# Performance work log

Measured on AMD Instinct MI355X. Metric: run time of the kernel, lower is better.

Reference implementation:

```python
import jax, jax.numpy as jnp
import numpy as np

EPS = 1e-5

def mean_variance_norm(x):
    # x: [b, c, h, w]; per-(b,c) instance norm over spatial, unbiased var (torch default)
    b, c, h, w = x.shape
    xf = x.reshape(b, c, h * w)
    mean = xf.mean(axis=2)
    var = xf.var(axis=2, ddof=1) + EPS
    std = jnp.sqrt(var)
    return (x - mean[:, :, None, None]) / std[:, :, None, None]

def conv1x1(x, w, b):
    # w: [out_c, in_c], b: [out_c]
    return jnp.einsum('oc,bchw->bohw', w, x) + b[None, :, None, None]

def setup_inputs() -> dict:
    key = jax.random.key(0)
    ks = jax.random.split(key, 10)
    b, C, H, W = 4, 512, 64, 64
    content = jax.random.normal(ks[0], (b, C, H, W), dtype=jnp.float32)
    style = jax.random.normal(ks[1], (b, C, H, W), dtype=jnp.float32)
    def w_(k, o, i):
        return jax.random.normal(k, (o, i), dtype=jnp.float32) * 0.02
    def b_(k, o):
        return jax.random.normal(k, (o,), dtype=jnp.float32) * 0.02
    return {
        'content': content, 'style': style,
        'f_w': w_(ks[2], C, C), 'f_b': b_(ks[3], C),
        'g_w': w_(ks[4], C, C), 'g_b': b_(ks[5], C),
        'h_w': w_(ks[6], C, C), 'h_b': b_(ks[7], C),
        'out_w': w_(ks[8], C, C), 'out_b': b_(ks[9], C),
    }

def reference(content, style, f_w, f_b, g_w, g_b, h_w, h_b, out_w, out_b):
    b, C, h, w = content.shape
    F = conv1x1(mean_variance_norm(content), f_w, f_b)   # [b,C,h,w]
    G = conv1x1(mean_variance_norm(style), g_w, g_b)     # [b,C,hg,wg]
    H = conv1x1(style, h_w, h_b)                          # [b,C,hg,wg]
    # spatial <= max_sample, so no subsampling branch
    Gf = G.reshape(b, C, -1)                              # [b,C,M]
    Hf = H.reshape(b, C, -1)                              # [b,C,M]
    Ff = F.reshape(b, C, -1)                              # [b,C,N]
    S = jnp.einsum('bcn,bcm->bnm', Ff, Gf)                # [b,N,M]
    S = jax.nn.softmax(S, axis=-1)
    styled = jnp.einsum('bcm,bnm->bcn', Hf, S)            # [b,C,N]
    styled = styled.reshape(b, C, h, w)
    return conv1x1(styled, out_w, out_b)
```

## Files before the change

kernel.cpp:

```cpp
#include <hip/hip_runtime.h>
#include <hip/hip_bf16.h>

typedef _Float16 f16;
typedef __attribute__((ext_vector_type(8))) _Float16 half8;
typedef __attribute__((ext_vector_type(4))) _Float16 half4;
typedef __attribute__((ext_vector_type(4))) float f32x4;

#define AS1 __attribute__((address_space(1)))
#define AS3 __attribute__((address_space(3)))

constexpr int CH  = 512;
constexpr int NSP = 4096;
constexpr int NB  = 4;

#define VM8  asm volatile("s_waitcnt vmcnt(8)"  ::: "memory")
#define VM6  asm volatile("s_waitcnt vmcnt(6)"  ::: "memory")
#define VM4  asm volatile("s_waitcnt vmcnt(4)"  ::: "memory")
#define VM2  asm volatile("s_waitcnt vmcnt(2)"  ::: "memory")
#define VM0  asm volatile("s_waitcnt vmcnt(0)"  ::: "memory")
#define BARS do { __builtin_amdgcn_s_barrier(); asm volatile("" ::: "memory"); } while (0)
#define SP1  __builtin_amdgcn_s_setprio(1)
#define SP0  __builtin_amdgcn_s_setprio(0)

__device__ __forceinline__ void gload_lds16(const void* g, void* l) {
    __builtin_amdgcn_global_load_lds((const AS1 void*)g, (AS3 void*)l, 16, 0, 0);
}

__global__ void transpose_f16_kernel(const float* __restrict__ content, const float* __restrict__ style,
                                     f16* __restrict__ content_t, f16* __restrict__ style_t,
                                     float* __restrict__ raw)
{
    int b = blockIdx.z & 3, is_style = blockIdx.z >> 2;
    const float* src = (is_style ? style : content) + (size_t)b * CH * NSP;
    f16* dst = (is_style ? style_t : content_t) + (size_t)b * NSP * CH;
    int c0 = blockIdx.y * 64, n0 = blockIdx.x * 64;
    __shared__ f16 tile[64][72];
    int t = threadIdx.x;
    #pragma unroll
    for (int i = 0; i < 4; i++) {
        int idx = t + i*256;
        int cr = idx >> 4, n4 = (idx & 15) * 4;
        float4 v = *(const float4*)(src + (size_t)(c0+cr)*NSP + n0 + n4);
        tile[cr][n4+0] = (f16)v.x; tile[cr][n4+1] = (f16)v.y;
        tile[cr][n4+2] = (f16)v.z; tile[cr][n4+3] = (f16)v.w;
    }
    __syncthreads();
    {
        int row = t >> 2, seg = (t & 3) * 16;
        float s1 = 0.f, s2 = 0.f;
        #pragma unroll
        for (int j = 0; j < 16; j++) {
            float x = (float)tile[row][seg + j];
            s1 += x; s2 += x * x;
        }
        s1 += __shfl_down(s1, 2, 4); s1 += __shfl_down(s1, 1, 4);
        s2 += __shfl_down(s2, 2, 4); s2 += __shfl_down(s2, 1, 4);
        if ((t & 3) == 0) {
            int si = is_style * 2 * NB * CH + b * CH + c0 + row;
            atomicAdd(&raw[si], s1);
            atomicAdd(&raw[si + NB * CH], s2);
        }
    }
    int nr = t >> 2, seg = (t & 3) * 16;
    __align__(16) f16 out_v[16];
    #pragma unroll
    for (int j = 0; j < 16; j++) out_v[j] = tile[seg + j][nr];
    f16* dp = dst + (size_t)(n0+nr)*CH + c0 + seg;
    *(int4*)dp = ((int4*)out_v)[0];
    *(int4*)(dp + 8) = ((int4*)out_v)[1];
}

__global__ void effw_kernel(const float* __restrict__ fw, const float* __restrict__ fb,
                            const float* __restrict__ gw, const float* __restrict__ gb,
                            const float* __restrict__ hw, const float* __restrict__ ow,
                            const float* __restrict__ raw,
                            f16* __restrict__ fw_e, float* __restrict__ fb_e,
                            f16* __restrict__ gw_e, float* __restrict__ gb_e,
                            f16* __restrict__ hw_h, f16* __restrict__ ow_h)
{
    int o = blockIdx.x, b = blockIdx.y, mode = blockIdx.z, t = threadIdx.x;
    if (mode >= 2) {
        if (b != 0) return;
        const float* srcw = (mode == 2) ? hw : ow;
        f16* dstw = (mode == 2) ? hw_h : ow_h;
        for (int c = t; c < CH; c += 128) dstw[o*CH + c] = (f16)srcw[o*CH + c];
        return;
    }
    const float* w  = mode ? gw : fw;
    const float* rw = raw + (mode ? 2*NB*CH : 0);
    f16* we = mode ? gw_e : fw_e;
    float part = 0.f;
    for (int c = t; c < CH; c += 128) {
        float s1 = rw[b*CH + c], s2 = rw[NB*CH + b*CH + c];
        float mn = s1 * (1.f/NSP);
        float var = (s2 - (float)NSP*mn*mn) * (1.f/(NSP-1));
        float is = rsqrtf(var + 1e-5f);
        float wv = w[o*CH + c];
        we[((size_t)b*CH + o)*CH + c] = (f16)(wv * is);
        part += wv * mn * is;
    }
    #pragma unroll
    for (int off = 32; off; off >>= 1) part += __shfl_down(part, off);
    __shared__ float rr[2];
    if ((t & 63) == 0) rr[t >> 6] = part;
    __syncthreads();
    if (t == 0) (mode ? gb_e : fb_e)[b*CH + o] = (mode ? gb : fb)[o] - (rr[0] + rr[1]);
}

__global__ __launch_bounds__(256)
void conv3_kernel(const f16* __restrict__ fw_e, const float* __restrict__ fb_e,
                  const f16* __restrict__ gw_e, const float* __restrict__ gb_e,
                  const f16* __restrict__ hw_h, const float* __restrict__ h_b,
                  const f16* __restrict__ content_t, const f16* __restrict__ style_t,
                  f16* __restrict__ F_t, f16* __restrict__ G_t, f16* __restrict__ H_)
{
    const int T = gridDim.x;
    const int bid = blockIdx.x;
    const int tile = (bid & 7) * (T >> 3) + (bid >> 3);
    const int zz = tile >> 7, rem = tile & 127;
    const int mt = rem >> 5, nt = rem & 31;
    const int kind = zz >> 2, b = zz & 3;

    const f16* W; const float* bias; const f16* Xt; f16* Y;
    if (kind == 0)      { W = fw_e + (size_t)b*CH*CH; bias = fb_e + b*CH; Xt = content_t + (size_t)b*NSP*CH; Y = F_t + (size_t)b*NSP*CH; }
    else if (kind == 1) { W = gw_e + (size_t)b*CH*CH; bias = gb_e + b*CH; Xt = style_t + (size_t)b*NSP*CH; Y = G_t + (size_t)b*NSP*CH; }
    else                { W = hw_h;                    bias = h_b;         Xt = style_t + (size_t)b*NSP*CH; Y = H_ + (size_t)b*CH*NSP; }

    const int m0 = mt * 128, n0 = nt * 128;
    const int t = threadIdx.x, wave = t >> 6, lane = t & 63;
    const int l15 = lane & 15, l4 = lane >> 4;
    const int wm = (wave >> 1) * 64, wn = (wave & 1) * 64;

    __shared__ __align__(16) f16 Al[8192];
    __shared__ __align__(16) f16 Bl[8192];

    f32x4 acc[4][4] = {};

    for (int ks = 0; ks < CH/64; ks++) {
        const int kk = ks * 64;
        #pragma unroll
        for (int j = 0; j < 4; j++) {
            int L  = ((wave*4 + j)*64 + lane) * 16;
            int SL = L ^ (((L >> 7) & 7) << 4);
            int row = SL >> 7, seg = (SL & 127) >> 1;
            gload_lds16(W  + (size_t)(m0 + row)*CH + kk + seg, &Al[L >> 1]);
            gload_lds16(Xt + (size_t)(n0 + row)*CH + kk + seg, &Bl[L >> 1]);
        }
        VM0; BARS;
        #pragma unroll
        for (int kb = 0; kb < 2; kb++) {
            half8 a[4], bb[4];
            #pragma unroll
            for (int i = 0; i < 4; i++) {
                int ab = (wm + i*16 + l15)*128 + kb*64 + l4*16;
                ab ^= ((ab >> 7) & 7) << 4;
                a[i] = *(const half8*)&Al[ab >> 1];
                int bby = (wn + i*16 + l15)*128 + kb*64 + l4*16;
                bby ^= ((bby >> 7) & 7) << 4;
                bb[i] = *(const half8*)&Bl[bby >> 1];
            }
            #pragma unroll
            for (int i = 0; i < 4; i++)
                #pragma unroll
                for (int jj = 0; jj < 4; jj++)
                    acc[i][jj] = __builtin_amdgcn_mfma_f32_16x16x32_f16(a[i], bb[jj], acc[i][jj], 0, 0, 0);
        }
        BARS;
    }

    #pragma unroll
    for (int i = 0; i < 4; i++) {
        const int ob = m0 + wm + i*16 + l4*4;
        f32x4 bv = *(const f32x4*)(bias + ob);
        #pragma unroll
        for (int jj = 0; jj < 4; jj++) {
            const int n = n0 + wn + jj*16 + l15;
            f32x4 v = acc[i][jj];
            v[0] += bv[0]; v[1] += bv[1]; v[2] += bv[2]; v[3] += bv[3];
            if (kind < 2) {
                half4 pk; pk[0]=(f16)v[0]; pk[1]=(f16)v[1]; pk[2]=(f16)v[2]; pk[3]=(f16)v[3];
                *(half4*)(Y + (size_t)n * CH + ob) = pk;
            } else {
                #pragma unroll
                for (int r = 0; r < 4; r++) Y[(size_t)(ob + r) * NSP + n] = (f16)v[r];
            }
        }
    }
}

template<int MODE>
__global__ __launch_bounds__(256)
void gemm_kernel(const f16* __restrict__ W, long wstrideb,
                 const f16* __restrict__ Xt, long xstrideb,
                 const float* __restrict__ bias, long bstrideb,
                 void* __restrict__ Y, long ystrideb,
                 int K, long ostride)
{
    const int z = blockIdx.z;
    W    += (size_t)z * wstrideb;
    Xt   += (size_t)z * xstrideb;
    bias += (size_t)z * bstrideb;
    const int m0 = blockIdx.y * 128, n0 = blockIdx.x * 128;
    const int t = threadIdx.x, wave = t >> 6, lane = t & 63;
    const int l15 = lane & 15, l4 = lane >> 4;
    const int wm = (wave >> 1) * 64, wn = (wave & 1) * 64;

    __shared__ __align__(16) f16 Al[2][8192];
    __shared__ __align__(16) f16 Bl[2][8192];

    f32x4 acc[4][4] = {};

    auto stage = [&](int bufi, int kk) {
        #pragma unroll
        for (int j = 0; j < 4; j++) {
            int L  = ((wave*4 + j)*64 + lane) * 16;
            int SL = L ^ (((L >> 7) & 7) << 4);
            int row = SL >> 7, seg = (SL & 127) >> 1;
            gload_lds16(W  + (size_t)(m0 + row)*K + kk + seg, &Al[bufi][L >> 1]);
            gload_lds16(Xt + (size_t)(n0 + row)*K + kk + seg, &Bl[bufi][L >> 1]);
        }
    };

    const int nks = K >> 6;
    stage(0, 0);
    for (int ks = 0; ks < nks; ks++) {
        int bufi = ks & 1;
        if (ks < nks-1) { stage(bufi ^ 1, (ks + 1) * 64); VM8; }
        else            { VM0; }
        BARS;
        #pragma unroll
        for (int kb = 0; kb < 2; kb++) {
            half8 a[4], bb[4];
            #pragma unroll
            for (int i = 0; i < 4; i++) {
                int ab = (wm + i*16 + l15)*128 + kb*64 + l4*16;
                ab ^= ((ab >> 7) & 7) << 4;
                a[i] = *(const half8*)&Al[bufi][ab >> 1];
                int bby = (wn + i*16 + l15)*128 + kb*64 + l4*16;
                bby ^= ((bby >> 7) & 7) << 4;
                bb[i] = *(const half8*)&Bl[bufi][bby >> 1];
            }
            #pragma unroll
            for (int i = 0; i < 4; i++)
                #pragma unroll
                for (int jj = 0; jj < 4; jj++)
                    acc[i][jj] = __builtin_amdgcn_mfma_f32_16x16x32_f16(a[i], bb[jj], acc[i][jj], 0, 0, 0);
        }
        BARS;
    }

    #pragma unroll
    for (int i = 0; i < 4; i++) {
        const int ob = m0 + wm + i*16 + l4*4;
        f32x4 bv = *(const f32x4*)(bias + ob);
        #pragma unroll
        for (int jj = 0; jj < 4; jj++) {
            const int n = n0 + wn + jj*16 + l15;
            f32x4 v = acc[i][jj];
            v[0] += bv[0]; v[1] += bv[1]; v[2] += bv[2]; v[3] += bv[3];
            float* Yf = (float*)Y + (size_t)z * ystrideb;
            #pragma unroll
            for (int r = 0; r < 4; r++) Yf[(size_t)(ob + r) * ostride + n] = v[r];
        }
    }
}

__global__ __launch_bounds__(256)
void out_fused_kernel(const f16* __restrict__ W, const f16* __restrict__ P0, const f16* __restrict__ P1,
                      const float* __restrict__ bias, float* __restrict__ Y)
{
    const int z = blockIdx.z;
    const f16* p0 = P0 + (size_t)z * NSP * CH;
    const f16* p1 = P1 + (size_t)z * NSP * CH;
    float* Yf = Y + (size_t)z * CH * NSP;
    const int m0 = blockIdx.y * 128, n0 = blockIdx.x * 128;
    const int t = threadIdx.x, wave = t >> 6, lane = t & 63;
    const int l15 = lane & 15, l4 = lane >> 4;
    const int wm = (wave >> 1) * 64, wn = (wave & 1) * 64;

    __shared__ __align__(16) f16 Al[8192];
    __shared__ __align__(16) f16 Bl[8192];

    f32x4 acc[4][4] = {};

    for (int ks = 0; ks < CH/64; ks++) {
        const int kk = ks * 64;
        int Ls[4];
        half8 b0[4], b1[4];
        #pragma unroll
        for (int j = 0; j < 4; j++) {
            int L  = ((wave*4 + j)*64 + lane) * 16;
            int SL = L ^ (((L >> 7) & 7) << 4);
            int row = SL >> 7, seg = (SL & 127) >> 1;
            gload_lds16(W + (size_t)(m0 + row)*CH + kk + seg, &Al[L >> 1]);
            b0[j] = *(const half8*)(p0 + (size_t)(n0 + row)*CH + kk + seg);
            b1[j] = *(const half8*)(p1 + (size_t)(n0 + row)*CH + kk + seg);
            Ls[j] = L;
        }
        #pragma unroll
        for (int j = 0; j < 4; j++) {
            half8 s;
            #pragma unroll
            for (int e = 0; e < 8; e++) s[e] = (f16)((float)b0[j][e] + (float)b1[j][e]);
            *(half8*)&Bl[Ls[j] >> 1] = s;
        }
        __syncthreads();
        #pragma unroll
        for (int kb = 0; kb < 2; kb++) {
            half8 a[4], bb[4];
            #pragma unroll
            for (int i = 0; i < 4; i++) {
                int ab = (wm + i*16 + l15)*128 + kb*64 + l4*16;
                ab ^= ((ab >> 7) & 7) << 4;
                a[i] = *(const half8*)&Al[ab >> 1];
                int bby = (wn + i*16 + l15)*128 + kb*64 + l4*16;
                bby ^= ((bby >> 7) & 7) << 4;
                bb[i] = *(const half8*)&Bl[bby >> 1];
            }
            #pragma unroll
            for (int i = 0; i < 4; i++)
                #pragma unroll
                for (int jj = 0; jj < 4; jj++)
                    acc[i][jj] = __builtin_amdgcn_mfma_f32_16x16x32_f16(a[i], bb[jj], acc[i][jj], 0, 0, 0);
        }
        __syncthreads();
    }

    #pragma unroll
    for (int i = 0; i < 4; i++) {
        const int ob = m0 + wm + i*16 + l4*4;
        f32x4 bv = *(const f32x4*)(bias + ob);
        #pragma unroll
        for (int jj = 0; jj < 4; jj++) {
            const int n = n0 + wn + jj*16 + l15;
            f32x4 v = acc[i][jj];
            #pragma unroll
            for (int r = 0; r < 4; r++) Yf[(size_t)(ob + r) * NSP + n] = v[r] + bv[r];
        }
    }
}

template<int TPB, int NCT>
__global__ __launch_bounds__(256)
void gemm_att_kernel(const f16* __restrict__ W, long wstrideb,
                     const f16* __restrict__ Xt, long xstrideb,
                     f16* __restrict__ Y, long ystrideb,
                     int K, long ostride)
{
    const int T = gridDim.x;
    const int bid = blockIdx.x;
    const int tile = (bid & 7) * (T >> 3) + (bid >> 3);
    const int z = tile / TPB, rem = tile - z * TPB;
    const int mt = rem / NCT, nt = rem - mt * NCT;
    W  += (size_t)z * wstrideb;
    Xt += (size_t)z * xstrideb;
    f16* Yb = Y + (size_t)z * ystrideb;
    const int m0 = mt * 128, n0 = nt * 128;

    const int t = threadIdx.x, wave = t >> 6, lane = t & 63;
    const int l15 = lane & 15, l4 = lane >> 4;
    const int wm = (wave >> 1) * 64, wn = (wave & 1) * 64;

    __shared__ __align__(16) f16 Al[8192];
    __shared__ __align__(16) f16 Bl[8192];

    f32x4 acc[4][4] = {};

    const int nks = K >> 6;
    for (int ks = 0; ks < nks; ks++) {
        const int kk = ks * 64;
        #pragma unroll
        for (int j = 0; j < 4; j++) {
            int L  = ((wave*4 + j)*64 + lane) * 16;
            int SL = L ^ (((L >> 7) & 7) << 4);
            int row = SL >> 7, seg = (SL & 127) >> 1;
            gload_lds16(W  + (size_t)(m0 + row)*K + kk + seg, &Al[L >> 1]);
            gload_lds16(Xt + (size_t)(n0 + row)*K + kk + seg, &Bl[L >> 1]);
        }
        VM0; BARS;
        #pragma unroll
        for (int kb = 0; kb < 2; kb++) {
            half8 a[4], bb[4];
            #pragma unroll
            for (int i = 0; i < 4; i++) {
                int ab = (wm + i*16 + l15)*128 + kb*64 + l4*16;
                ab ^= ((ab >> 7) & 7) << 4;
                a[i] = *(const half8*)&Al[ab >> 1];
                int bby = (wn + i*16 + l15)*128 + kb*64 + l4*16;
                bby ^= ((bby >> 7) & 7) << 4;
                bb[i] = *(const half8*)&Bl[bby >> 1];
            }
            #pragma unroll
            for (int i = 0; i < 4; i++)
                #pragma unroll
                for (int jj = 0; jj < 4; jj++)
                    acc[i][jj] = __builtin_amdgcn_mfma_f32_16x16x32_f16(a[i], bb[jj], acc[i][jj], 0, 0, 0);
        }
        BARS;
    }

    #pragma unroll
    for (int i = 0; i < 4; i++) {
        const int ob = m0 + wm + i*16 + l4*4;
        #pragma unroll
        for (int jj = 0; jj < 4; jj++) {
            const int ncol = n0 + wn + jj*16 + l15;
            #pragma unroll
            for (int r = 0; r < 4; r++)
                Yb[(size_t)(ob + r) * ostride + ncol] = (f16)acc[i][jj][r];
        }
    }
}

template<int TPB, int NCT, int SPLITK>
__global__ __launch_bounds__(512)
void gemm256_kernel(const f16* __restrict__ W, long wstrideb,
                    const f16* __restrict__ Xt, long xstrideb,
                    f16* __restrict__ Y0, f16* __restrict__ Y1, long ystrideb,
                    int K, int kstride, long ostride)
{
    const int T = gridDim.x;
    const int bid = blockIdx.x;
    const int tile = (bid & 7) * (T >> 3) + (bid >> 3);
    int rem = tile, sp = 0;
    if constexpr (SPLITK == 2) { sp = tile / (NB * TPB); rem = tile - sp * NB * TPB; }
    const int z = rem / TPB; rem -= z * TPB;
    const int mt = rem / NCT, nt = rem - mt * NCT;
    const f16* Wb = W  + (size_t)z * wstrideb + (size_t)sp * K;
    const f16* Xb = Xt + (size_t)z * xstrideb + (size_t)sp * K;
    f16* Yb = ((SPLITK == 2 && sp) ? Y1 : Y0) + (size_t)z * ystrideb;
    const int m0 = mt * 256, n0 = nt * 256;

    const int t = threadIdx.x, lane = t & 63, wave = t >> 6;
    const int l15 = lane & 15, l4 = lane >> 4;
    const int wr = wave >> 2, wc = wave & 3;

    __shared__ __align__(16) f16 As[2][16384];
    __shared__ __align__(16) f16 Bs[2][16384];

    f32x4 acc[8][4] = {};

    auto stA = [&](int nbuf, int kk, int half, int q) {
        int L  = half*16384 + q*8192 + t*16;
        int SL = L ^ (((L >> 7) & 7) << 4);
        gload_lds16(Wb + (size_t)(m0 + (SL >> 7)) * kstride + kk + ((SL & 127) >> 1), &As[nbuf][L >> 1]);
    };
    auto stB = [&](int nbuf, int kk, int half, int q) {
        int L  = half*16384 + q*8192 + t*16;
        int SL = L ^ (((L >> 7) & 7) << 4);
        gload_lds16(Xb + (size_t)(n0 + (SL >> 7)) * kstride + kk + ((SL & 127) >> 1), &Bs[nbuf][L >> 1]);
    };
    auto ldA = [&](int buf, int i, int kb) {
        int L = (((i&3)*16) + wr*64 + ((i>>2)*128) + l15)*128 + kb*64 + l4*16;
        L ^= ((L >> 7) & 7) << 4;
        return *(const half8*)&As[buf][L >> 1];
    };
    auto ldB = [&](int buf, int j, int kb) {
        int L = (((j&1)*16) + wc*32 + ((j>>1)*128) + l15)*128 + kb*64 + l4*16;
        L ^= ((L >> 7) & 7) << 4;
        return *(const half8*)&Bs[buf][L >> 1];
    };

    const int nks = K >> 6;
    stA(0,0,0,0); stA(0,0,0,1);
    stB(0,0,0,0); stB(0,0,0,1);
    stB(0,0,1,0); stB(0,0,1,1);
    stA(0,0,1,0); stA(0,0,1,1);
    VM4;
    if (nks > 1) {
        stA(1,64,0,0); stA(1,64,0,1);
        stB(1,64,0,0); stB(1,64,0,1);
        stB(1,64,1,0); stB(1,64,1,1);
        VM6;
    } else { VM0; }
    BARS;

    half8 a[4][2], b01[2][2], b23[2][2];

    for (int kt = 0; kt < nks; kt++) {
        const int buf = kt & 1;
        const int kk1 = (kt+1) << 6, kk2 = (kt+2) << 6;
        const bool s1 = (kt+1 < nks), s2 = (kt+2 < nks);

        #pragma unroll
        for (int i = 0; i < 4; i++) { a[i][0] = ldA(buf, i, 0); a[i][1] = ldA(buf, i, 1); }
        #pragma unroll
        for (int j = 0; j < 2; j++) { b01[j][0] = ldB(buf, j, 0); b01[j][1] = ldB(buf, j, 1); }
        if (s1) { stA(buf^1, kk1, 1, 0); stA(buf^1, kk1, 1, 1); }
        else    { VM2; }
        BARS; SP1;
        #pragma unroll
        for (int i = 0; i < 4; i++)
            #pragma unroll
            for (int j = 0; j < 2; j++)
                #pragma unroll
                for (int kb = 0; kb < 2; kb++)
                    acc[i][j] = __builtin_amdgcn_mfma_f32_16x16x32_f16(a[i][kb], b01[j][kb], acc[i][j], 0, 0, 0);
        SP0; BARS;

        #pragma unroll
        for (int j = 0; j < 2; j++) { b23[j][0] = ldB(buf, 2+j, 0); b23[j][1] = ldB(buf, 2+j, 1); }
        if (s2)       { stA(buf, kk2, 0, 0); stA(buf, kk2, 0, 1); }
        else if (!s1) { VM0; }
        BARS; SP1;
        #pragma unroll
        for (int i = 0; i < 4; i++)
            #pragma unroll
            for (int j = 0; j < 2; j++)
                #pragma unroll
                for (int kb = 0; kb < 2; kb++)
                    acc[i][2+j] = __builtin_amdgcn_mfma_f32_16x16x32_f16(a[i][kb], b23[j][kb], acc[i][2+j], 0, 0, 0);
        SP0; BARS;

        #pragma unroll
        for (int i = 0; i < 4; i++) { a[i][0] = ldA(buf, 4+i, 0); a[i][1] = ldA(buf, 4+i, 1); }
        if (s2) { stB(buf, kk2, 0, 0); stB(buf, kk2, 0, 1); }
        BARS; SP1;
        #pragma unroll
        for (int i = 0; i < 4; i++)
            #pragma unroll
            for (int j = 0; j < 2; j++)
                #pragma unroll
                for (int kb = 0; kb < 2; kb++)
                    acc[4+i][2+j] = __builtin_amdgcn_mfma_f32_16x16x32_f16(a[i][kb], b23[j][kb], acc[4+i][2+j], 0, 0, 0);
        SP0; BARS;

        if (s2)      { stB(buf, kk2, 1, 0); stB(buf, kk2, 1, 1); VM6; }
        else if (s1) { VM4; }
        BARS; SP1;
        #pragma unroll
        for (int i = 0; i < 4; i++)
            #pragma unroll
            for (int j = 0; j < 2; j++)
                #pragma unroll
                for (int kb = 0; kb < 2; kb++)
                    acc[4+i][j] = __builtin_amdgcn_mfma_f32_16x16x32_f16(a[i][kb], b01[j][kb], acc[4+i][j], 0, 0, 0);
        SP0; BARS;
    }

    #pragma unroll
    for (int i = 0; i < 8; i++) {
        const int ob = m0 + ((i&3)*16) + wr*64 + ((i>>2)*128) + l4*4;
        #pragma unroll
        for (int j = 0; j < 4; j++) {
            const int ncol = n0 + ((j&1)*16) + wc*32 + ((j>>1)*128) + l15;
            f32x4 v = acc[i][j];
            #pragma unroll
            for (int r = 0; r < 4; r++)
                Yb[(size_t)(ob + r) * ostride + ncol] = (f16)v[r];
        }
    }
}

__global__ __launch_bounds__(256)
void softmax_kernel(f16* __restrict__ S, int nrows)
{
    int row = blockIdx.x * 4 + (threadIdx.x >> 6);
    if (row >= nrows) return;
    int lane = threadIdx.x & 63;
    f16* p = S + (size_t)row * NSP + lane * 8;

    half8 v[8];
    #pragma unroll
    for (int j = 0; j < 8; j++) v[j] = *(const half8*)(p + j * 512);

    float mx = -1e30f;
    #pragma unroll
    for (int j = 0; j < 8; j++)
        #pragma unroll
        for (int e = 0; e < 8; e++) mx = fmaxf(mx, (float)v[j][e]);
    #pragma unroll
    for (int off = 32; off; off >>= 1) mx = fmaxf(mx, __shfl_xor(mx, off));

    float ex[64];
    float s = 0.f;
    #pragma unroll
    for (int j = 0; j < 8; j++)
        #pragma unroll
        for (int e = 0; e < 8; e++) {
            float x = __expf((float)v[j][e] - mx);
            ex[j*8 + e] = x; s += x;
        }
    #pragma unroll
    for (int off = 32; off; off >>= 1) s += __shfl_xor(s, off);
    float inv = 1.0f / s;

    #pragma unroll
    for (int j = 0; j < 8; j++) {
        half8 o;
        #pragma unroll
        for (int e = 0; e < 8; e++) o[e] = (f16)(ex[j*8 + e] * inv);
        *(half8*)(p + j * 512) = o;
    }
}

extern "C" void kernel_launch(void* const* d_in, const int* in_sizes, int n_in,
                              void* d_out, int out_size, void* d_ws, size_t ws_size,
                              hipStream_t stream)
{
    const float* content = (const float*)d_in[0];
    const float* style   = (const float*)d_in[1];
    const float* f_w = (const float*)d_in[2];
    const float* f_b = (const float*)d_in[3];
    const float* g_w = (const float*)d_in[4];
    const float* g_b = (const float*)d_in[5];
    const float* h_w = (const float*)d_in[6];
    const float* h_b = (const float*)d_in[7];
    const float* o_w = (const float*)d_in[8];
    const float* o_b = (const float*)d_in[9];

    char* ws = (char*)d_ws;
    size_t off = 0;
    auto alloc = [&](size_t bytes) -> void* {
        void* p = ws + off;
        off += (bytes + 255) & ~(size_t)255;
        return p;
    };
    float* raw = (float*)alloc(4 * NB*CH * 4);
    f16* fw_e = (f16*)alloc((size_t)NB*CH*CH*2);
    f16* gw_e = (f16*)alloc((size_t)NB*CH*CH*2);
    f16* hw_h = (f16*)alloc((size_t)CH*CH*2);
    f16* ow_h = (f16*)alloc((size_t)CH*CH*2);
    float* fb_e = (float*)alloc((size_t)NB*CH*4);
    float* gb_e = (float*)alloc((size_t)NB*CH*4);
    f16* content_t = (f16*)alloc((size_t)NB*NSP*CH*2);
    f16* style_t   = (f16*)alloc((size_t)NB*NSP*CH*2);
    f16* F_t = (f16*)alloc((size_t)NB*NSP*CH*2);
    f16* G_t = (f16*)alloc((size_t)NB*NSP*CH*2);
    f16* H_  = (f16*)alloc((size_t)NB*CH*NSP*2);
    f16* styled_t = content_t;

    size_t s_plane = (size_t)NSP * NSP;
    bool all4 = (off + 4 * s_plane * 2 <= ws_size);
    f16* S16 = (f16*)alloc((all4 ? 4 : 1) * s_plane * 2);
    if (off > ws_size) return;

    hipMemsetAsync(raw, 0, 4 * NB*CH * 4, stream);
    transpose_f16_kernel<<<dim3(NSP/64, CH/64, NB*2), dim3(256), 0, stream>>>(
        content, style, content_t, style_t, raw);
    effw_kernel<<<dim3(CH, NB, 4), dim3(128), 0, stream>>>(f_w, f_b, g_w, g_b, h_w, o_w, raw,
                                                           fw_e, fb_e, gw_e, gb_e, hw_h, ow_h);
    conv3_kernel<<<dim3(12*128), dim3(256), 0, stream>>>(
        fw_e, fb_e, gw_e, gb_e, hw_h, h_b, content_t, style_t, F_t, G_t, H_);

    if (all4) {
        gemm256_kernel<256,16,1><<<dim3(1024), dim3(512), 0, stream>>>(
            F_t, (long)NSP*CH, G_t, (long)NSP*CH, S16, nullptr, (long)s_plane, CH, CH, (long)NSP);
        softmax_kernel<<<dim3(NB*NSP/4), dim3(256), 0, stream>>>(S16, NB*NSP);
        gemm256_kernel<32,2,2><<<dim3(256), dim3(512), 0, stream>>>(
            S16, (long)s_plane, H_, (long)CH*NSP, F_t, G_t, (long)NSP*CH, NSP/2, NSP, (long)CH);
        out_fused_kernel<<<dim3(NSP/128, CH/128, NB), dim3(256), 0, stream>>>(
            ow_h, F_t, G_t, o_b, (float*)d_out);
    } else {
        for (int b = 0; b < NB; b++) {
            gemm_att_kernel<1024,32><<<dim3(1024), dim3(256), 0, stream>>>(
                F_t + (size_t)b*NSP*CH, 0L, G_t + (size_t)b*NSP*CH, 0L,
                S16, 0L, CH, (long)NSP);
            softmax_kernel<<<dim3(NSP/4), dim3(256), 0, stream>>>(S16, NSP);
            gemm_att_kernel<128,4><<<dim3(128), dim3(256), 0, stream>>>(
                S16, 0L, H_ + (size_t)b*CH*NSP, 0L,
                styled_t + (size_t)b*NSP*CH, 0L, NSP, (long)CH);
        }
        gemm_kernel<2><<<dim3(NSP/128, CH/128, NB), dim3(256), 0, stream>>>(
            ow_h, 0L, styled_t, (long)NSP*CH, o_b, 0L, d_out, (long)CH*NSP, CH, (long)NSP);
    }
}
```

Baseline: 286.2 us.

## Fuse softmax exponentiation into PV GEMM and defer normalization to output

Replaces the in-place softmax pass with a read-only max/sum kernel that stores per-row max and inverse sum. The PV GEMM now applies exp(s - max) to the S tiles as it reads them from LDS, and the output projection multiplies by the inverse sum while combining the split-K partials. This removes the write-back of the full f16 S matrix, but adds many exp operations inside the GEMM's LDS-read path. That may slow the MFMA loop, and the unnormalized f16 accumulation changes precision.

```diff
diff --git a/kernel.cpp b/kernel.cpp
--- a/kernel.cpp
+++ b/kernel.cpp
@@ -267,11 +267,13 @@
 
 __global__ __launch_bounds__(256)
 void out_fused_kernel(const f16* __restrict__ W, const f16* __restrict__ P0, const f16* __restrict__ P1,
+                      const float* __restrict__ linv,
                       const float* __restrict__ bias, float* __restrict__ Y)
 {
     const int z = blockIdx.z;
     const f16* p0 = P0 + (size_t)z * NSP * CH;
     const f16* p1 = P1 + (size_t)z * NSP * CH;
+    const float* li = linv + (size_t)z * NSP;
     float* Yf = Y + (size_t)z * CH * NSP;
     const int m0 = blockIdx.y * 128, n0 = blockIdx.x * 128;
     const int t = threadIdx.x, wave = t >> 6, lane = t & 63;
@@ -287,6 +289,7 @@
         const int kk = ks * 64;
         int Ls[4];
         half8 b0[4], b1[4];
+        float lv[4];
         #pragma unroll
         for (int j = 0; j < 4; j++) {
             int L  = ((wave*4 + j)*64 + lane) * 16;
@@ -295,13 +298,14 @@
             gload_lds16(W + (size_t)(m0 + row)*CH + kk + seg, &Al[L >> 1]);
             b0[j] = *(const half8*)(p0 + (size_t)(n0 + row)*CH + kk + seg);
             b1[j] = *(const half8*)(p1 + (size_t)(n0 + row)*CH + kk + seg);
+            lv[j] = li[n0 + row];
             Ls[j] = L;
         }
         #pragma unroll
         for (int j = 0; j < 4; j++) {
             half8 s;
             #pragma unroll
-            for (int e = 0; e < 8; e++) s[e] = (f16)((float)b0[j][e] + (float)b1[j][e]);
+            for (int e = 0; e < 8; e++) s[e] = (f16)(((float)b0[j][e] + (float)b1[j][e]) * lv[j]);
             *(half8*)&Bl[Ls[j] >> 1] = s;
         }
         __syncthreads();
@@ -412,12 +416,13 @@
     }
 }
 
-template<int TPB, int NCT, int SPLITK>
+template<int TPB, int NCT, int SPLITK, int EXPA = 0>
 __global__ __launch_bounds__(512)
 void gemm256_kernel(const f16* __restrict__ W, long wstrideb,
                     const f16* __restrict__ Xt, long xstrideb,
                     f16* __restrict__ Y0, f16* __restrict__ Y1, long ystrideb,
-                    int K, int kstride, long ostride)
+                    int K, int kstride, long ostride,
+                    const float* __restrict__ MX)
 {
     const int T = gridDim.x;
     const int bid = blockIdx.x;
@@ -439,6 +444,13 @@
     __shared__ __align__(16) f16 Bs[2][16384];
 
     f32x4 acc[8][4] = {};
+
+    float mxv[8];
+    if constexpr (EXPA) {
+        #pragma unroll
+        for (int i = 0; i < 8; i++)
+            mxv[i] = MX[(size_t)z * NSP + m0 + ((i&3)*16) + wr*64 + ((i>>2)*128) + l15];
+    }
 
     auto stA = [&](int nbuf, int kk, int half, int q) {
         int L  = half*16384 + q*8192 + t*16;
@@ -453,7 +465,14 @@
     auto ldA = [&](int buf, int i, int kb) {
         int L = (((i&3)*16) + wr*64 + ((i>>2)*128) + l15)*128 + kb*64 + l4*16;
         L ^= ((L >> 7) & 7) << 4;
-        return *(const half8*)&As[buf][L >> 1];
+        half8 v = *(const half8*)&As[buf][L >> 1];
+        if constexpr (EXPA) {
+            half8 r;
+            #pragma unroll
+            for (int e = 0; e < 8; e++) r[e] = (f16)__expf((float)v[e] - mxv[i]);
+            return r;
+        }
+        return v;
     };
     auto ldB = [&](int buf, int j, int kb) {
         int L = (((j&1)*16) + wc*32 + ((j>>1)*128) + l15)*128 + kb*64 + l4*16;
@@ -553,6 +572,40 @@
 }
 
 __global__ __launch_bounds__(256)
+void maxsum_kernel(const f16* __restrict__ S, float* __restrict__ MX, float* __restrict__ LI, int nrows)
+{
+    int row = blockIdx.x * 4 + (threadIdx.x >> 6);
+    if (row >= nrows) return;
+    int lane = threadIdx.x & 63;
+    const f16* p = S + (size_t)row * NSP + lane * 8;
+
+    half8 v[8];
+    #pragma unroll
+    for (int j = 0; j < 8; j++) v[j] = *(const half8*)(p + j * 512);
+
+    float mx = -1e30f;
+    #pragma unroll
+    for (int j = 0; j < 8; j++)
+        #pragma unroll
+        for (int e = 0; e < 8; e++) mx = fmaxf(mx, (float)v[j][e]);
+    #pragma unroll
+    for (int off = 32; off; off >>= 1) mx = fmaxf(mx, __shfl_xor(mx, off));
+
+    float s = 0.f;
+    #pragma unroll
+    for (int j = 0; j < 8; j++)
+        #pragma unroll
+        for (int e = 0; e < 8; e++) s += __expf((float)v[j][e] - mx);
+    #pragma unroll
+    for (int off = 32; off; off >>= 1) s += __shfl_xor(s, off);
+
+    if (lane == 0) {
+        MX[row] = mx;
+        LI[row] = 1.0f / s;
+    }
+}
+
+__global__ __launch_bounds__(256)
 void softmax_kernel(f16* __restrict__ S, int nrows)
 {
     int row = blockIdx.x * 4 + (threadIdx.x >> 6);
@@ -617,6 +670,8 @@
         return p;
     };
     float* raw = (float*)alloc(4 * NB*CH * 4);
+    float* MX  = (float*)alloc((size_t)NB*NSP*4);
+    float* LI  = (float*)alloc((size_t)NB*NSP*4);
     f16* fw_e = (f16*)alloc((size_t)NB*CH*CH*2);
     f16* gw_e = (f16*)alloc((size_t)NB*CH*CH*2);
     f16* hw_h = (f16*)alloc((size_t)CH*CH*2);
@@ -645,12 +700,12 @@
 
     if (all4) {
         gemm256_kernel<256,16,1><<<dim3(1024), dim3(512), 0, stream>>>(
-            F_t, (long)NSP*CH, G_t, (long)NSP*CH, S16, nullptr, (long)s_plane, CH, CH, (long)NSP);
-        softmax_kernel<<<dim3(NB*NSP/4), dim3(256), 0, stream>>>(S16, NB*NSP);
-        gemm256_kernel<32,2,2><<<dim3(256), dim3(512), 0, stream>>>(
-            S16, (long)s_plane, H_, (long)CH*NSP, F_t, G_t, (long)NSP*CH, NSP/2, NSP, (long)CH);
+            F_t, (long)NSP*CH, G_t, (long)NSP*CH, S16, nullptr, (long)s_plane, CH, CH, (long)NSP, nullptr);
+        maxsum_kernel<<<dim3(NB*NSP/4), dim3(256), 0, stream>>>(S16, MX, LI, NB*NSP);
+        gemm256_kernel<32,2,2,1><<<dim3(256), dim3(512), 0, stream>>>(
+            S16, (long)s_plane, H_, (long)CH*NSP, F_t, G_t, (long)NSP*CH, NSP/2, NSP, (long)CH, MX);
         out_fused_kernel<<<dim3(NSP/128, CH/128, NB), dim3(256), 0, stream>>>(
-            ow_h, F_t, G_t, o_b, (float*)d_out);
+            ow_h, F_t, G_t, LI, o_b, (float*)d_out);
     } else {
         for (int b = 0; b < NB; b++) {
             gemm_att_kernel<1024,32><<<dim3(1024), dim3(256), 0, stream>>>(
```

Result: slower. 340.5 us (+19.0%).
